# Optimization experiments

Hardware: AMD Instinct MI355X
Metric: run time of the kernel (lower is better)

The kernel has to match this reference:

```python
import jax, jax.numpy as jnp
import numpy as np

C = 1024
B = 32
N = 512
H = W = 32
SUB = (256, 64)
K = (16, 16)
OUT = 3584
LN_EPS = 1e-5


def setup_inputs() -> dict:
    key = jax.random.key(0)
    ks = jax.random.split(key, 12)
    s = 0.02
    C2 = C + 2
    inp = {}
    inp["points"] = jax.random.uniform(ks[0], (B, N, 2), jnp.float32)
    inp["feat_map"] = jax.random.normal(ks[1], (C, H, W), jnp.float32)
    for i in range(2):
        inp[f"diff_w{i}"] = jax.random.normal(ks[2 + 4 * i], (C2, C2), jnp.float32) * s
        inp[f"diff_b{i}"] = jnp.zeros((C2,), jnp.float32)
        inp[f"agg_w{i}"] = jax.random.normal(ks[3 + 4 * i], (C, 2 * C2), jnp.float32) * s
        inp[f"agg_b{i}"] = jnp.zeros((C,), jnp.float32)
        inp[f"ln_g{i}"] = jnp.ones((C,), jnp.float32)
        inp[f"ln_b{i}"] = jnp.zeros((C,), jnp.float32)
    inp["flat_w"] = jax.random.normal(ks[10], (C, C * SUB[-1]), jnp.float32) * s
    inp["flat_b"] = jnp.zeros((C,), jnp.float32)
    inp["dim_w"] = jax.random.normal(ks[11], (OUT, C), jnp.float32) * s
    inp["dim_b"] = jnp.zeros((OUT,), jnp.float32)
    return inp


def _bilinear(feat, xy):
    # feat [C,H,W]; xy [P,2] grid coords in [-1,1], (x,y) order, align_corners=True
    Cc, Hh, Ww = feat.shape
    x = (xy[:, 0] + 1.0) * 0.5 * (Ww - 1)
    y = (xy[:, 1] + 1.0) * 0.5 * (Hh - 1)
    x0 = jnp.floor(x)
    y0 = jnp.floor(y)
    wx = x - x0
    wy = y - y0
    x0i = jnp.clip(x0, 0, Ww - 1).astype(jnp.int32)
    x1i = jnp.clip(x0 + 1, 0, Ww - 1).astype(jnp.int32)
    y0i = jnp.clip(y0, 0, Hh - 1).astype(jnp.int32)
    y1i = jnp.clip(y0 + 1, 0, Hh - 1).astype(jnp.int32)
    f00 = feat[:, y0i, x0i]
    f01 = feat[:, y0i, x1i]
    f10 = feat[:, y1i, x0i]
    f11 = feat[:, y1i, x1i]
    out = (f00 * (1 - wx) * (1 - wy) + f01 * wx * (1 - wy)
           + f10 * (1 - wx) * wy + f11 * wx * wy)
    return out.T  # [P,C]


def _fps(pts, n):
    # iterative farthest point sampling; pts [Np,2] -> indices [n]
    Np = pts.shape[0]

    def body(carry, _):
        dist, far = carry
        d = jnp.sum((pts - pts[far]) ** 2, axis=-1)
        dist = jnp.minimum(dist, d)
        nxt = jnp.argmax(dist).astype(jnp.int32)
        return (dist, nxt), far

    init = (jnp.full((Np,), 1e10, pts.dtype), jnp.int32(0))
    (_, _), idx = jax.lax.scan(body, init, None, length=n)
    return idx


def _stage(points, feats, n_sub, k, dw, db, aw, ab, lg, lb):
    # FPS downsample
    fps_idx = jax.vmap(lambda p: _fps(p, n_sub))(points)              # [B,S]
    new_pts = jnp.take_along_axis(points, fps_idx[..., None], axis=1)  # [B,S,2]
    new_fts = jnp.take_along_axis(feats, fps_idx[..., None], axis=1)   # [B,S,C]
    # brute-force KNN
    d2 = jnp.sum((new_pts[:, :, None, :] - points[:, None, :, :]) ** 2, axis=-1)  # [B,S,N]
    _, nn_idx = jax.lax.top_k(-d2, k)                                   # [B,S,K]
    gp = jax.vmap(lambda p, i: p[i])(points, nn_idx)                    # [B,S,K,2]
    gf = jax.vmap(lambda f, i: f[i])(feats, nn_idx)                     # [B,S,K,C]
    anchor = jnp.concatenate([new_fts, new_pts], axis=-1)[:, :, None, :]  # [B,S,1,C+2]
    diff = jnp.concatenate([gf, gp], axis=-1) - anchor
    diff = diff @ dw.T + db                                             # diff projector
    gath = jnp.concatenate([diff, jnp.broadcast_to(anchor, diff.shape)], axis=-1)  # [B,S,K,2(C+2)]
    h = jax.nn.relu(jnp.einsum('bskd,cd->bskc', gath, aw) + ab)         # 1x1 conv + relu
    mu = jnp.mean(h, axis=-1, keepdims=True)
    var = jnp.var(h, axis=-1, keepdims=True)
    h = (h - mu) * jax.lax.rsqrt(var + LN_EPS) * lg + lb                # layernorm over C
    return new_pts, jnp.max(h, axis=2)                                  # max-pool over neighbors


def _forward(points, feat_map, dw0, db0, aw0, ab0, lg0, lb0,
             dw1, db1, aw1, ab1, lg1, lb1, fw, fb, dmw, dmb):
    Bp, Np = points.shape[0], points.shape[1]
    grid = 2.0 * points[..., ::-1] - 1.0            # flip (row,col) -> (x,y), to [-1,1]
    fts = _bilinear(feat_map, grid.reshape(-1, 2)).reshape(Bp, Np, -1)
    pts = points
    pts, fts = _stage(pts, fts, SUB[0], K[0], dw0, db0, aw0, ab0, lg0, lb0)
    pts, fts = _stage(pts, fts, SUB[1], K[1], dw1, db1, aw1, ab1, lg1, lb1)
    flat = fts.reshape(Bp, -1)
    return (flat @ fw.T + fb) @ dmw.T + dmb


def reference(points, feat_map, diff_w0, diff_b0, agg_w0, agg_b0, ln_g0, ln_b0,
              diff_w1, diff_b1, agg_w1, agg_b1, ln_g1, ln_b1,
              flat_w, flat_b, dim_w, dim_b):
    return _forward(points, feat_map, diff_w0, diff_b0, agg_w0, agg_b0, ln_g0, ln_b0,
                    diff_w1, diff_b1, agg_w1, agg_b1, ln_g1, ln_b1,
                    flat_w, flat_b, dim_w, dim_b)
```

## Files before the change

kernel.cpp:

```cpp
#include <hip/hip_runtime.h>
#include <cstdint>
#include <cstddef>

static const int B_ = 32, N_ = 512, C_ = 1024, C2_ = 1026, CC2_ = 2052;
static const int S0_ = 256, S1_ = 64, K_ = 16, OUT_ = 3584;
static const int LDP_ = 1152;

typedef unsigned short ushort;
typedef __attribute__((ext_vector_type(8))) short short8;
typedef __attribute__((ext_vector_type(4))) float f32x4;

__device__ __forceinline__ ushort f2bf(float x) {
  unsigned u = __float_as_uint(x);
  unsigned r = (u + 0x7fffu + ((u >> 16) & 1u)) >> 16;
  return (ushort)r;
}
__device__ __forceinline__ float bf2f(ushort b) {
  return __uint_as_float(((unsigned)b) << 16);
}

__device__ __forceinline__ void gload16(const void* g, void* l) {
  __builtin_amdgcn_global_load_lds((const __attribute__((address_space(1))) void*)g,
                                   (__attribute__((address_space(3))) void*)l, 16, 0, 0);
}

__device__ __forceinline__ unsigned wave_umax_dpp(unsigned v) {
  unsigned t;
  t = (unsigned)__builtin_amdgcn_update_dpp(0, (int)v, 0x111, 0xf, 0xf, true);
  v = v > t ? v : t;
  t = (unsigned)__builtin_amdgcn_update_dpp(0, (int)v, 0x112, 0xf, 0xf, true);
  v = v > t ? v : t;
  t = (unsigned)__builtin_amdgcn_update_dpp(0, (int)v, 0x114, 0xf, 0xf, true);
  v = v > t ? v : t;
  t = (unsigned)__builtin_amdgcn_update_dpp(0, (int)v, 0x118, 0xf, 0xf, true);
  v = v > t ? v : t;
  t = (unsigned)__builtin_amdgcn_update_dpp(0, (int)v, 0x142, 0xf, 0xf, true);
  v = v > t ? v : t;
  t = (unsigned)__builtin_amdgcn_update_dpp(0, (int)v, 0x143, 0xf, 0xf, true);
  v = v > t ? v : t;
  return v;
}

template <int OMODE>
__device__ __forceinline__ void dev_mgemm(int bx, int by, ushort* As, ushort* Bs, int M, int Neff,
                                          int K, const ushort* __restrict__ A, int lda,
                                          const int* __restrict__ rowidx,
                                          const ushort* __restrict__ Wt, int ldw,
                                          const float* __restrict__ bias,
                                          void* __restrict__ Cout, int ldc) {
  int t = threadIdx.x;
  int w = t >> 6, l = t & 63;
  int row0 = by * 128, col0 = bx * 128;
  f32x4 acc[4][4];
#pragma unroll
  for (int i = 0; i < 4; i++)
#pragma unroll
    for (int j = 0; j < 4; j++) acc[i][j] = (f32x4){0.f, 0.f, 0.f, 0.f};

  int srow = l >> 2;
  int scol = (l & 3) * 8;
  int ar0 = min(row0 + w * 16 + srow, M - 1);
  int ar1 = min(row0 + 64 + w * 16 + srow, M - 1);
  if (rowidx) { ar0 = rowidx[ar0]; ar1 = rowidx[ar1]; }
  const ushort* gA0 = A + (size_t)ar0 * lda + scol;
  const ushort* gA1 = A + (size_t)ar1 * lda + scol;
  const ushort* gB0 = Wt + (size_t)(col0 + w * 16 + srow) * ldw + scol;
  const ushort* gB1 = Wt + (size_t)(col0 + 64 + w * 16 + srow) * ldw + scol;
  ushort* lA0 = As + w * 512;
  ushort* lA1 = As + 2048 + w * 512;
  ushort* lB0 = Bs + w * 512;
  ushort* lB1 = Bs + 2048 + w * 512;

  int wm = w >> 1, wn = w & 1;
  int fr = l & 15, fg = l >> 4;

  for (int kt = 0; kt < K; kt += 64) {
    __syncthreads();
    gload16(gA0 + kt, lA0);
    gload16(gA1 + kt, lA1);
    gload16(gB0 + kt, lB0);
    gload16(gB1 + kt, lB1);
    gload16(gA0 + kt + 32, lA0 + 4096);
    gload16(gA1 + kt + 32, lA1 + 4096);
    gload16(gB0 + kt + 32, lB0 + 4096);
    gload16(gB1 + kt + 32, lB1 + 4096);
    __syncthreads();
#pragma unroll
    for (int ks = 0; ks < 2; ks++) {
      short8 af[4], bf[4];
#pragma unroll
      for (int mi = 0; mi < 4; mi++)
        af[mi] = *(const short8*)&As[ks * 4096 + (wm * 64 + mi * 16 + fr) * 32 + fg * 8];
#pragma unroll
      for (int ni = 0; ni < 4; ni++)
        bf[ni] = *(const short8*)&Bs[ks * 4096 + (wn * 64 + ni * 16 + fr) * 32 + fg * 8];
#pragma unroll
      for (int mi = 0; mi < 4; mi++)
#pragma unroll
        for (int ni = 0; ni < 4; ni++)
          acc[mi][ni] =
              __builtin_amdgcn_mfma_f32_16x16x32_bf16(af[mi], bf[ni], acc[mi][ni], 0, 0, 0);
    }
  }

  ushort* C = (ushort*)Cout;
  if (OMODE == 1) {
#pragma unroll
    for (int mi = 0; mi < 4; mi++)
#pragma unroll
      for (int ni = 0; ni < 4; ni++)
#pragma unroll
        for (int q = 0; q < 4; q++) {
          int r = row0 + wm * 64 + mi * 16 + fg * 4 + q;
          int c = col0 + wn * 64 + ni * 16 + fr;
          if (r < M) C[(size_t)r * ldc + c] = f2bf(c < Neff ? acc[mi][ni][q] : 0.f);
        }
  } else {
#pragma unroll
    for (int mi = 0; mi < 4; mi++)
#pragma unroll
      for (int ni = 0; ni < 4; ni++)
#pragma unroll
        for (int q = 0; q < 4; q++) {
          int r = row0 + wm * 64 + mi * 16 + fg * 4 + q;
          int c = col0 + wn * 64 + ni * 16 + fr;
          if (r < M) C[(size_t)r * ldc + c] = f2bf(acc[mi][ni][q] + bias[c]);
        }
  }
}

template <int NPL>
__device__ __forceinline__ void dev_fps(int b, int Np, int nsub, const float* __restrict__ pts,
                                        int stride, int* __restrict__ rows) {
  __builtin_amdgcn_s_setprio(3);
  int lane = threadIdx.x;
  const float* pb = pts + (size_t)b * Np * stride;
  float px[NPL], py[NPL], dist[NPL];
#pragma unroll
  for (int i = 0; i < NPL; i++) {
    int j = lane + 64 * i;
    px[i] = pb[(size_t)j * stride + 0];
    py[i] = pb[(size_t)j * stride + 1];
    dist[i] = 1e10f;
  }
  int far = 0;
  float fx = pb[0], fy = pb[1];
  for (int s = 0; s < nsub; s++) {
    if (lane == 0) rows[b * nsub + s] = b * Np + far;
    unsigned bd = 0;
    int bidx = lane;
#pragma unroll
    for (int i = 0; i < NPL; i++) {
      float dx = __fsub_rn(px[i], fx), dy = __fsub_rn(py[i], fy);
      float d = __fadd_rn(__fmul_rn(dx, dx), __fmul_rn(dy, dy));
      dist[i] = fminf(dist[i], d);
      unsigned db = __float_as_uint(dist[i]);
      if (i == 0) {
        bd = db;
      } else if (db > bd) {
        bd = db;
        bidx = lane + 64 * i;
      }
    }
    unsigned maxd = (unsigned)__builtin_amdgcn_readlane((int)wave_umax_dpp(bd), 63);
    unsigned cand = (bd == maxd) ? ~(unsigned)bidx : 0u;
    far = (int)~(unsigned)__builtin_amdgcn_readlane((int)wave_umax_dpp(cand), 63);
    int chunk = far >> 6, owner = far & 63;
    float cx = px[0], cy = py[0];
#pragma unroll
    for (int i = 1; i < NPL; i++) {
      bool cnd = (chunk == i);
      cx = cnd ? px[i] : cx;
      cy = cnd ? py[i] : cy;
    }
    fx = __uint_as_float((unsigned)__builtin_amdgcn_readlane((int)__float_as_uint(cx), owner));
    fy = __uint_as_float((unsigned)__builtin_amdgcn_readlane((int)__float_as_uint(cy), owner));
  }
  __builtin_amdgcn_s_setprio(0);
}

template <int NPL>
__device__ __forceinline__ void dev_knn(int bs, int S, int Np, const float* __restrict__ pts,
                                        int stride, const int* __restrict__ rows,
                                        int* __restrict__ nn) {
  int b = bs / S;
  int lane = threadIdx.x & 63;
  const float* pb = pts + (size_t)b * Np * stride;
  int arow = rows[bs];
  float ax = pts[(size_t)arow * stride + 0];
  float ay = pts[(size_t)arow * stride + 1];
  float d2[NPL];
#pragma unroll
  for (int i = 0; i < NPL; i++) {
    int j = lane + 64 * i;
    float dx = __fsub_rn(ax, pb[(size_t)j * stride + 0]);
    float dy = __fsub_rn(ay, pb[(size_t)j * stride + 1]);
    d2[i] = __fadd_rn(__fmul_rn(dx, dx), __fmul_rn(dy, dy));
  }
  unsigned mask = 0;
  for (int k = 0; k < K_; k++) {
    float bv = INFINITY;
    int bi = 0x7fffffff;
#pragma unroll
    for (int i = 0; i < NPL; i++) {
      int j = lane + 64 * i;
      bool used = (mask >> i) & 1u;
      if (!used && (d2[i] < bv || (d2[i] == bv && j < bi))) { bv = d2[i]; bi = j; }
    }
#pragma unroll
    for (int off = 32; off; off >>= 1) {
      float ov = __shfl_xor(bv, off);
      int oi = __shfl_xor(bi, off);
      if (ov < bv || (ov == bv && oi < bi)) { bv = ov; bi = oi; }
    }
    if ((bi & 63) == lane) mask |= 1u << (bi >> 6);
    if (lane == 0) nn[bs * K_ + k] = b * Np + bi;
  }
}

__device__ __forceinline__ void dev_bilinear(int r, const float* __restrict__ points,
                                             const float* __restrict__ fmT,
                                             ushort* __restrict__ X0) {
  float p0 = points[r * 2 + 0], p1 = points[r * 2 + 1];
  float g0 = __fsub_rn(__fmul_rn(2.0f, p1), 1.0f);
  float g1 = __fsub_rn(__fmul_rn(2.0f, p0), 1.0f);
  float x = __fmul_rn(__fmul_rn(__fadd_rn(g0, 1.0f), 0.5f), 31.0f);
  float y = __fmul_rn(__fmul_rn(__fadd_rn(g1, 1.0f), 0.5f), 31.0f);
  float x0f = floorf(x), y0f = floorf(y);
  float wx = __fsub_rn(x, x0f), wy = __fsub_rn(y, y0f);
  int x0i = (int)fminf(fmaxf(x0f, 0.f), 31.f);
  int x1i = (int)fminf(fmaxf(__fadd_rn(x0f, 1.f), 0.f), 31.f);
  int y0i = (int)fminf(fmaxf(y0f, 0.f), 31.f);
  int y1i = (int)fminf(fmaxf(__fadd_rn(y0f, 1.f), 0.f), 31.f);
  float omwx = __fsub_rn(1.f, wx), omwy = __fsub_rn(1.f, wy);
  size_t i00 = (size_t)(y0i * 32 + x0i) * 1024;
  size_t i01 = (size_t)(y0i * 32 + x1i) * 1024;
  size_t i10 = (size_t)(y1i * 32 + x0i) * 1024;
  size_t i11 = (size_t)(y1i * 32 + x1i) * 1024;
  int t = threadIdx.x;
  int c0 = t * 4;
  ushort* xr = X0 + (size_t)r * LDP_;
  float4 f00 = *(const float4*)(fmT + i00 + c0);
  float4 f01 = *(const float4*)(fmT + i01 + c0);
  float4 f10 = *(const float4*)(fmT + i10 + c0);
  float4 f11 = *(const float4*)(fmT + i11 + c0);
  float a[4] = {f00.x, f00.y, f00.z, f00.w};
  float b[4] = {f01.x, f01.y, f01.z, f01.w};
  float c[4] = {f10.x, f10.y, f10.z, f10.w};
  float d[4] = {f11.x, f11.y, f11.z, f11.w};
  ushort o[4];
#pragma unroll
  for (int i = 0; i < 4; i++) {
    float t1 = a[i] * omwx * omwy;
    float t2 = b[i] * wx * omwy;
    float t3 = c[i] * omwx * wy;
    float t4 = d[i] * wx * wy;
    o[i] = f2bf(((t1 + t2) + t3) + t4);
  }
  uint2 uv = {(unsigned)o[0] | ((unsigned)o[1] << 16), (unsigned)o[2] | ((unsigned)o[3] << 16)};
  *(uint2*)(xr + c0) = uv;
  if (t == 0) { xr[1024] = f2bf(p0); xr[1025] = f2bf(p1); }
  if (t < 126) xr[1026 + t] = 0;
}

static const int PREP_CVT = 2304;
static const int PREP_TT = 1296;
static const int PREP_FMT = 1024;
static const int PREP_TOTAL = 4 * PREP_CVT + 2 * PREP_TT + 512 + PREP_FMT;

__global__ __launch_bounds__(256) void k_prep(
    const float* __restrict__ aw0, const float* __restrict__ aw1, const float* __restrict__ dw0,
    const float* __restrict__ dw1, const float* __restrict__ db0, const float* __restrict__ ab0,
    const float* __restrict__ db1, const float* __restrict__ ab1,
    const float* __restrict__ feat_map, ushort* __restrict__ awdb0, ushort* __restrict__ awab0,
    ushort* __restrict__ awdb1, ushort* __restrict__ awab1, ushort* __restrict__ dwT0,
    ushort* __restrict__ dwT1, float* __restrict__ dvp0, float* __restrict__ dvp1,
    float* __restrict__ fmT) {
  __shared__ float tile[32][33];
  int bid = blockIdx.x;
  if (bid < 4 * PREP_CVT) {
    int job = bid / PREP_CVT, lb = bid % PREP_CVT;
    const float* src = (job < 2) ? aw0 : aw1;
    int soff = (job & 1) ? C2_ : 0;
    ushort* dst = (job == 0) ? awdb0 : (job == 1) ? awab0 : (job == 2) ? awdb1 : awab1;
    unsigned e = (lb * 256u + threadIdx.x) * 2u;
    unsigned r = e / (unsigned)LDP_, c = e % (unsigned)LDP_;
    float v0 = 0.f, v1 = 0.f;
    const float* sp = src + (size_t)r * CC2_ + soff + c;
    if ((int)c < C2_) v0 = sp[0];
    if ((int)(c + 1) < C2_) v1 = sp[1];
    *(unsigned*)(dst + e) = (unsigned)f2bf(v0) | ((unsigned)f2bf(v1) << 16);
    return;
  }
  bid -= 4 * PREP_CVT;
  if (bid < 2 * PREP_TT) {
    int which = bid / PREP_TT, id = bid % PREP_TT;
    const float* src = which ? dw1 : dw0;
    ushort* dst = which ? dwT1 : dwT0;
    int bx = (id % 36) * 32, by = (id / 36) * 32;
    int tx = threadIdx.x & 31, ty4 = (threadIdx.x >> 5) * 4;
#pragma unroll
    for (int i = 0; i < 4; i++) {
      int r = by + ty4 + i, c = bx + tx;
      tile[ty4 + i][tx] = (r < C2_ && c < C2_) ? src[(size_t)r * C2_ + c] : 0.f;
    }
    __syncthreads();
#pragma unroll
    for (int i = 0; i < 4; i++)
      dst[(size_t)(bx + ty4 + i) * LDP_ + by + tx] = f2bf(tile[tx][ty4 + i]);
    return;
  }
  bid -= 2 * PREP_TT;
  if (bid < 512) {
    int which = bid >> 8;
    int cb = bid & 255;
    const float* aw = which ? aw1 : aw0;
    const float* db = which ? db1 : db0;
    const float* ab = which ? ab1 : ab0;
    float* dvp = which ? dvp1 : dvp0;
    int w = threadIdx.x >> 6, lane = threadIdx.x & 63;
    int c = cb * 4 + w;
    const float* wr = aw + (size_t)c * CC2_;
    float s = 0.f;
    for (int d = lane; d < C2_; d += 64) s += db[d] * wr[d];
#pragma unroll
    for (int off = 32; off; off >>= 1) s += __shfl_xor(s, off);
    if (lane == 0) dvp[c] = ab[c] + s;
    return;
  }
  bid -= 512;
  {
    int yx0 = (bid & 31) * 32, c0 = (bid >> 5) * 32;
    int tx = threadIdx.x & 31, ty = threadIdx.x >> 5;
#pragma unroll
    for (int i = 0; i < 4; i++)
      tile[ty + 8 * i][tx] = feat_map[(size_t)(c0 + ty + 8 * i) * 1024 + yx0 + tx];
    __syncthreads();
#pragma unroll
    for (int i = 0; i < 4; i++)
      fmT[(size_t)(yx0 + ty + 8 * i) * 1024 + c0 + tx] = tile[tx][ty + 8 * i];
  }
}

__global__ __launch_bounds__(256) void k_wc_bil(
    const ushort* __restrict__ awdb0, const ushort* __restrict__ dwT0, ushort* __restrict__ Wcb0,
    const ushort* __restrict__ awdb1, const ushort* __restrict__ dwT1, ushort* __restrict__ Wcb1,
    const float* __restrict__ points, const float* __restrict__ fmT, ushort* __restrict__ Xb0) {
  __shared__ ushort As[8192];
  __shared__ ushort Bs[8192];
  int bid = blockIdx.x;
  if (bid < 72) {
    dev_mgemm<1>(bid / 8, bid % 8, As, Bs, C_, C2_, LDP_, awdb0, LDP_, nullptr, dwT0, LDP_,
                 nullptr, Wcb0, LDP_);
  } else if (bid < 144) {
    int b2 = bid - 72;
    dev_mgemm<1>(b2 / 8, b2 % 8, As, Bs, C_, C2_, LDP_, awdb1, LDP_, nullptr, dwT1, LDP_, nullptr,
                 Wcb1, LDP_);
  } else {
    dev_bilinear(bid - 144, points, fmT, Xb0);
  }
}

template <int NPL>
__global__ __launch_bounds__(256) void k_gemm_fps(int nrb, int Mg, const ushort* __restrict__ A,
                                                  int lda, const ushort* __restrict__ Wt,
                                                  ushort* __restrict__ Gout, int Np, int nsub,
                                                  const float* __restrict__ pts, int stride,
                                                  int* __restrict__ rows) {
  __shared__ ushort As[8192];
  __shared__ ushort Bs[8192];
  int bid = blockIdx.x;
  if (bid < 32) {
    if (threadIdx.x < 64) dev_fps<NPL>(bid, Np, nsub, pts, stride, rows);
    return;
  }
  int b2 = bid - 32;
  dev_mgemm<1>(b2 / nrb, b2 % nrb, As, Bs, Mg, C_, LDP_, A, lda, nullptr, Wt, LDP_, nullptr, Gout,
               C_);
}

template <int NPL>
__global__ __launch_bounds__(256) void k_gemm_knn(int nrb, int Mp, const ushort* __restrict__ A,
                                                  int lda, const int* __restrict__ rowsA,
                                                  const ushort* __restrict__ Wt,
                                                  const float* __restrict__ bias,
                                                  ushort* __restrict__ Pout, int ngemm, int S,
                                                  int Np, const float* __restrict__ pts,
                                                  int stride, const int* __restrict__ rows,
                                                  int* __restrict__ nn) {
  __shared__ ushort As[8192];
  __shared__ ushort Bs[8192];
  int bid = blockIdx.x;
  if (bid < ngemm) {
    dev_mgemm<2>(bid / nrb, bid % nrb, As, Bs, Mp, C_, LDP_, A, lda, rowsA, Wt, LDP_, bias, Pout,
                 C_);
  } else {
    int w = threadIdx.x >> 6;
    int qid = (bid - ngemm) * 4 + w;
    dev_knn<NPL>(qid, S, Np, pts, stride, rows, nn);
  }
}

__global__ __launch_bounds__(256) void k_flat(const ushort* __restrict__ A,
                                              const float* __restrict__ W,
                                              float* __restrict__ Cp) {
  int t = threadIdx.x;
  int w = t >> 6, l = t & 63;
  int fr = l & 15, fg = l >> 4;
  int col0 = blockIdx.x * 128 + w * 32;
  size_t k0 = (size_t)blockIdx.z * 2048;
  f32x4 acc[2][2];
#pragma unroll
  for (int i = 0; i < 2; i++)
#pragma unroll
    for (int j = 0; j < 2; j++) acc[i][j] = (f32x4){0.f, 0.f, 0.f, 0.f};
  const ushort* a0 = A + (size_t)fr * 65536 + k0 + fg * 8;
  const ushort* a1 = A + (size_t)(16 + fr) * 65536 + k0 + fg * 8;
  const float* b0 = W + (size_t)(col0 + fr) * 65536 + k0 + fg * 8;
  const float* b1 = W + (size_t)(col0 + 16 + fr) * 65536 + k0 + fg * 8;
  for (int kt = 0; kt < 2048; kt += 32) {
    short8 af0 = *(const short8*)(a0 + kt);
    short8 af1 = *(const short8*)(a1 + kt);
    float4 p0 = *(const float4*)(b0 + kt);
    float4 p1 = *(const float4*)(b0 + kt + 4);
    float4 q0 = *(const float4*)(b1 + kt);
    float4 q1 = *(const float4*)(b1 + kt + 4);
    short8 bf0, bf1;
    bf0[0] = (short)f2bf(p0.x); bf0[1] = (short)f2bf(p0.y);
    bf0[2] = (short)f2bf(p0.z); bf0[3] = (short)f2bf(p0.w);
    bf0[4] = (short)f2bf(p1.x); bf0[5] = (short)f2bf(p1.y);
    bf0[6] = (short)f2bf(p1.z); bf0[7] = (short)f2bf(p1.w);
    bf1[0] = (short)f2bf(q0.x); bf1[1] = (short)f2bf(q0.y);
    bf1[2] = (short)f2bf(q0.z); bf1[3] = (short)f2bf(q0.w);
    bf1[4] = (short)f2bf(q1.x); bf1[5] = (short)f2bf(q1.y);
    bf1[6] = (short)f2bf(q1.z); bf1[7] = (short)f2bf(q1.w);
    acc[0][0] = __builtin_amdgcn_mfma_f32_16x16x32_bf16(af0, bf0, acc[0][0], 0, 0, 0);
    acc[1][0] = __builtin_amdgcn_mfma_f32_16x16x32_bf16(af1, bf0, acc[1][0], 0, 0, 0);
    acc[0][1] = __builtin_amdgcn_mfma_f32_16x16x32_bf16(af0, bf1, acc[0][1], 0, 0, 0);
    acc[1][1] = __builtin_amdgcn_mfma_f32_16x16x32_bf16(af1, bf1, acc[1][1], 0, 0, 0);
  }
  float* Cz = Cp + (size_t)blockIdx.z * 32 * 1024;
#pragma unroll
  for (int mi = 0; mi < 2; mi++)
#pragma unroll
    for (int ni = 0; ni < 2; ni++)
#pragma unroll
      for (int q = 0; q < 4; q++) {
        int r = mi * 16 + fg * 4 + q;
        int c = col0 + ni * 16 + fr;
        Cz[(size_t)r * 1024 + c] = acc[mi][ni][q];
      }
}

__global__ __launch_bounds__(256) void k_dim(const ushort* __restrict__ A,
                                             const float* __restrict__ W,
                                             float* __restrict__ Cp) {
  int t = threadIdx.x;
  int w = t >> 6, l = t & 63;
  int fr = l & 15, fg = l >> 4;
  int col0 = blockIdx.x * 128 + w * 32;
  int k0 = blockIdx.z * 256;
  f32x4 acc[2][2];
#pragma unroll
  for (int i = 0; i < 2; i++)
#pragma unroll
    for (int j = 0; j < 2; j++) acc[i][j] = (f32x4){0.f, 0.f, 0.f, 0.f};
  const ushort* a0 = A + (size_t)fr * 1024 + k0 + fg * 8;
  const ushort* a1 = A + (size_t)(16 + fr) * 1024 + k0 + fg * 8;
  const float* b0 = W + (size_t)(col0 + fr) * 1024 + k0 + fg * 8;
  const float* b1 = W + (size_t)(col0 + 16 + fr) * 1024 + k0 + fg * 8;
  for (int kt = 0; kt < 256; kt += 32) {
    short8 af0 = *(const short8*)(a0 + kt);
    short8 af1 = *(const short8*)(a1 + kt);
    float4 p0 = *(const float4*)(b0 + kt);
    float4 p1 = *(const float4*)(b0 + kt + 4);
    float4 q0 = *(const float4*)(b1 + kt);
    float4 q1 = *(const float4*)(b1 + kt + 4);
    short8 bf0, bf1;
    bf0[0] = (short)f2bf(p0.x); bf0[1] = (short)f2bf(p0.y);
    bf0[2] = (short)f2bf(p0.z); bf0[3] = (short)f2bf(p0.w);
    bf0[4] = (short)f2bf(p1.x); bf0[5] = (short)f2bf(p1.y);
    bf0[6] = (short)f2bf(p1.z); bf0[7] = (short)f2bf(p1.w);
    bf1[0] = (short)f2bf(q0.x); bf1[1] = (short)f2bf(q0.y);
    bf1[2] = (short)f2bf(q0.z); bf1[3] = (short)f2bf(q0.w);
    bf1[4] = (short)f2bf(q1.x); bf1[5] = (short)f2bf(q1.y);
    bf1[6] = (short)f2bf(q1.z); bf1[7] = (short)f2bf(q1.w);
    acc[0][0] = __builtin_amdgcn_mfma_f32_16x16x32_bf16(af0, bf0, acc[0][0], 0, 0, 0);
    acc[1][0] = __builtin_amdgcn_mfma_f32_16x16x32_bf16(af1, bf0, acc[1][0], 0, 0, 0);
    acc[0][1] = __builtin_amdgcn_mfma_f32_16x16x32_bf16(af0, bf1, acc[0][1], 0, 0, 0);
    acc[1][1] = __builtin_amdgcn_mfma_f32_16x16x32_bf16(af1, bf1, acc[1][1], 0, 0, 0);
  }
  float* Cz = Cp + (size_t)blockIdx.z * 32 * 3584;
#pragma unroll
  for (int mi = 0; mi < 2; mi++)
#pragma unroll
    for (int ni = 0; ni < 2; ni++)
#pragma unroll
      for (int q = 0; q < 4; q++) {
        int r = mi * 16 + fg * 4 + q;
        int c = col0 + ni * 16 + fr;
        Cz[(size_t)r * 3584 + c] = acc[mi][ni][q];
      }
}

__global__ __launch_bounds__(256) void k_fused_stage(
    const ushort* __restrict__ G, const ushort* __restrict__ Pb, const int* __restrict__ rows,
    const int* __restrict__ nn, const float* __restrict__ lng, const float* __restrict__ lnb,
    const float* __restrict__ prev_pts, int pts_stride, ushort* __restrict__ Xout, int ld_out,
    float* __restrict__ coords_out) {
  __shared__ float sm[4][1024];
  int chunk = (int)gridDim.x >> 3;
  int bs = (blockIdx.x & 7) * chunk + (blockIdx.x >> 3);
  int t = threadIdx.x;
  int w = t >> 6, lane = t & 63;
  int c0 = lane * 16;
  int arow = rows[bs];
  float base[16], lg[16], lb[16], acc[16];
  {
    short8 pA = *(const short8*)(Pb + (size_t)bs * C_ + c0);
    short8 pB = *(const short8*)(Pb + (size_t)bs * C_ + c0 + 8);
    short8 gA = *(const short8*)(G + (size_t)arow * C_ + c0);
    short8 gB = *(const short8*)(G + (size_t)arow * C_ + c0 + 8);
#pragma unroll
    for (int i = 0; i < 8; i++) {
      base[i] = bf2f((ushort)pA[i]) - bf2f((ushort)gA[i]);
      base[8 + i] = bf2f((ushort)pB[i]) - bf2f((ushort)gB[i]);
    }
#pragma unroll
    for (int i = 0; i < 4; i++) {
      float4 gv = *(const float4*)(lng + c0 + 4 * i);
      float4 bv = *(const float4*)(lnb + c0 + 4 * i);
      lg[4 * i] = gv.x; lg[4 * i + 1] = gv.y; lg[4 * i + 2] = gv.z; lg[4 * i + 3] = gv.w;
      lb[4 * i] = bv.x; lb[4 * i + 1] = bv.y; lb[4 * i + 2] = bv.z; lb[4 * i + 3] = bv.w;
      acc[4 * i] = -INFINITY; acc[4 * i + 1] = -INFINITY;
      acc[4 * i + 2] = -INFINITY; acc[4 * i + 3] = -INFINITY;
    }
  }
#pragma unroll
  for (int kk = 0; kk < 4; kk++) {
    int g = nn[bs * K_ + w * 4 + kk];
    const ushort* Gr = G + (size_t)g * C_ + c0;
    short8 xA = *(const short8*)(Gr);
    short8 xB = *(const short8*)(Gr + 8);
    float v[16];
    float s1 = 0.f, s2 = 0.f;
#pragma unroll
    for (int i = 0; i < 8; i++) {
      float x = fmaxf(bf2f((ushort)xA[i]) + base[i], 0.f);
      v[i] = x; s1 += x; s2 += x * x;
      float y = fmaxf(bf2f((ushort)xB[i]) + base[8 + i], 0.f);
      v[8 + i] = y; s1 += y; s2 += y * y;
    }
#pragma unroll
    for (int off = 32; off; off >>= 1) {
      s1 += __shfl_xor(s1, off);
      s2 += __shfl_xor(s2, off);
    }
    float mu = s1 * (1.f / 1024.f);
    float var = s2 * (1.f / 1024.f) - mu * mu;
    float rstd = 1.f / sqrtf(var + 1e-5f);
#pragma unroll
    for (int i = 0; i < 16; i++) {
      float nv = (v[i] - mu) * rstd * lg[i] + lb[i];
      acc[i] = fmaxf(acc[i], nv);
    }
  }
#pragma unroll
  for (int i = 0; i < 16; i += 4) {
    f32x4 av = {acc[i], acc[i + 1], acc[i + 2], acc[i + 3]};
    *(f32x4*)&sm[w][c0 + i] = av;
  }
  __syncthreads();
  {
    int cc = t * 4;
    f32x4 m0 = *(const f32x4*)&sm[0][cc];
    f32x4 m1 = *(const f32x4*)&sm[1][cc];
    f32x4 m2 = *(const f32x4*)&sm[2][cc];
    f32x4 m3 = *(const f32x4*)&sm[3][cc];
    ushort o[4];
#pragma unroll
    for (int j = 0; j < 4; j++)
      o[j] = f2bf(fmaxf(fmaxf(m0[j], m1[j]), fmaxf(m2[j], m3[j])));
    uint2 uv = {(unsigned)o[0] | ((unsigned)o[1] << 16), (unsigned)o[2] | ((unsigned)o[3] << 16)};
    *(uint2*)(Xout + (size_t)bs * ld_out + cc) = uv;
  }
  if (prev_pts) {
    float p0 = prev_pts[(size_t)arow * pts_stride + 0];
    float p1 = prev_pts[(size_t)arow * pts_stride + 1];
    if (t == 0) {
      Xout[(size_t)bs * ld_out + 1024] = f2bf(p0);
      Xout[(size_t)bs * ld_out + 1025] = f2bf(p1);
      coords_out[bs * 2 + 0] = p0;
      coords_out[bs * 2 + 1] = p1;
    }
    if (t < 126) Xout[(size_t)bs * ld_out + 1026 + t] = 0;
  }
}

template <int OUTBF>
__global__ __launch_bounds__(256) void k_reduce(int total, int Ncols, int nz,
                                                const float* __restrict__ part,
                                                const float* __restrict__ bias,
                                                void* __restrict__ out) {
  int i = blockIdx.x * 256 + threadIdx.x;
  if (i >= total) return;
  float s = bias[i % Ncols];
  for (int z = 0; z < nz; z++) s += part[(size_t)z * total + i];
  if (OUTBF)
    ((ushort*)out)[i] = f2bf(s);
  else
    ((float*)out)[i] = s;
}

extern "C" void kernel_launch(void* const* d_in, const int* in_sizes, int n_in, void* d_out,
                              int out_size, void* d_ws, size_t ws_size, hipStream_t stream) {
  (void)in_sizes; (void)n_in; (void)out_size; (void)ws_size;
  const float* points = (const float*)d_in[0];
  const float* feat_map = (const float*)d_in[1];
  const float* dw0 = (const float*)d_in[2];
  const float* db0 = (const float*)d_in[3];
  const float* aw0 = (const float*)d_in[4];
  const float* ab0 = (const float*)d_in[5];
  const float* lg0 = (const float*)d_in[6];
  const float* lb0 = (const float*)d_in[7];
  const float* dw1 = (const float*)d_in[8];
  const float* db1 = (const float*)d_in[9];
  const float* aw1 = (const float*)d_in[10];
  const float* ab1 = (const float*)d_in[11];
  const float* lg1 = (const float*)d_in[12];
  const float* lb1 = (const float*)d_in[13];
  const float* fw = (const float*)d_in[14];
  const float* fb = (const float*)d_in[15];
  const float* dmw = (const float*)d_in[16];
  const float* dmb = (const float*)d_in[17];
  float* out = (float*)d_out;

  char* wsb = (char*)d_ws;
  size_t off = 0;
  auto alloc = [&](size_t bytes) -> void* {
    void* p = wsb + off;
    off = (off + bytes + 255) & ~(size_t)255;
    return p;
  };
  float* fmT = (float*)alloc((size_t)1024 * 1024 * 4);
  ushort* Xb0 = (ushort*)alloc((size_t)B_ * N_ * LDP_ * 2);
  ushort* Gb = (ushort*)alloc((size_t)B_ * N_ * C_ * 2);
  ushort* Pb = (ushort*)alloc((size_t)B_ * S0_ * C_ * 2);
  ushort* Xb1 = (ushort*)alloc((size_t)B_ * S0_ * LDP_ * 2);
  ushort* fts2b = (ushort*)alloc((size_t)B_ * S1_ * C_ * 2);
  float* coords1 = (float*)alloc((size_t)B_ * S0_ * 2 * 4);
  ushort* awdb0 = (ushort*)alloc((size_t)C_ * LDP_ * 2);
  ushort* awab0 = (ushort*)alloc((size_t)C_ * LDP_ * 2);
  ushort* awdb1 = (ushort*)alloc((size_t)C_ * LDP_ * 2);
  ushort* awab1 = (ushort*)alloc((size_t)C_ * LDP_ * 2);
  ushort* dwT0 = (ushort*)alloc((size_t)LDP_ * LDP_ * 2);
  ushort* dwT1 = (ushort*)alloc((size_t)LDP_ * LDP_ * 2);
  ushort* Wcb0 = (ushort*)alloc((size_t)C_ * LDP_ * 2);
  ushort* Wcb1 = (ushort*)alloc((size_t)C_ * LDP_ * 2);
  float* dvp0 = (float*)alloc(1024 * 4);
  float* dvp1 = (float*)alloc(1024 * 4);
  int* rows0 = (int*)alloc(B_ * S0_ * 4);
  int* nn0 = (int*)alloc(B_ * S0_ * K_ * 4);
  int* rows1 = (int*)alloc(B_ * S1_ * 4);
  int* nn1 = (int*)alloc(B_ * S1_ * K_ * 4);
  float* hpart = (float*)alloc((size_t)32 * B_ * C_ * 4);
  ushort* hidb = (ushort*)alloc((size_t)B_ * C_ * 2);
  float* opart = (float*)alloc((size_t)4 * B_ * OUT_ * 4);

  k_prep<<<PREP_TOTAL, 256, 0, stream>>>(aw0, aw1, dw0, dw1, db0, ab0, db1, ab1, feat_map, awdb0,
                                         awab0, awdb1, awab1, dwT0, dwT1, dvp0, dvp1, fmT);
  k_wc_bil<<<144 + B_ * N_, 256, 0, stream>>>(awdb0, dwT0, Wcb0, awdb1, dwT1, Wcb1, points, fmT,
                                              Xb0);
  k_gemm_fps<8><<<32 + 1024, 256, 0, stream>>>(128, B_ * N_, Xb0, LDP_, Wcb0, Gb, N_, S0_, points,
                                               2, rows0);
  k_gemm_knn<8><<<512 + (B_ * S0_) / 4, 256, 0, stream>>>(64, B_ * S0_, Xb0, LDP_, rows0, awab0,
                                                          dvp0, Pb, 512, S0_, N_, points, 2,
                                                          rows0, nn0);
  k_fused_stage<<<B_ * S0_, 256, 0, stream>>>(Gb, Pb, rows0, nn0, lg0, lb0, points, 2, Xb1, LDP_,
                                              coords1);
  k_gemm_fps<4><<<32 + 512, 256, 0, stream>>>(64, B_ * S0_, Xb1, LDP_, Wcb1, Gb, S0_, S1_,
                                              coords1, 2, rows1);
  k_gemm_knn<4><<<128 + (B_ * S1_) / 4, 256, 0, stream>>>(16, B_ * S1_, Xb1, LDP_, rows1, awab1,
                                                          dvp1, Pb, 128, S1_, S0_, coords1, 2,
                                                          rows1, nn1);
  k_fused_stage<<<B_ * S1_, 256, 0, stream>>>(Gb, Pb, rows1, nn1, lg1, lb1, nullptr, 0, fts2b, C_,
                                              nullptr);
  {
    dim3 g(8, 1, 32);
    k_flat<<<g, 256, 0, stream>>>(fts2b, fw, hpart);
  }
  k_reduce<1><<<(B_ * C_ + 255) / 256, 256, 0, stream>>>(B_ * C_, C_, 32, hpart, fb, hidb);
  {
    dim3 g(28, 1, 4);
    k_dim<<<g, 256, 0, stream>>>(hidb, dmw, opart);
  }
  k_reduce<0><<<(B_ * OUT_ + 255) / 256, 256, 0, stream>>>(B_ * OUT_, OUT_, 4, opart, dmb, out);
}
```

Baseline: 474.0 us.

## Pre-convert flat_w to bf16 inside stage-0 kernels and drop k_dim split-K

Adds extra blocks to the stage-0 gemm_fps and gemm_knn launches that convert the 256 MB fp32 flat_w into a 128 MB bf16 workspace copy. k_flat can then stream half the bytes from that copy, and the conversion overlaps with the latency-bound FPS/KNN work. Separately, k_dim no longer splits K four ways; it writes out directly with the bias added, which removes the partial buffer and the final reduce launch. The cost is an extra full read of flat_w plus a bf16 write each call, and k_dim now runs on only 28 blocks.

```diff
diff --git a/kernel.cpp b/kernel.cpp
--- a/kernel.cpp
+++ b/kernel.cpp
@@ -39,6 +39,19 @@
   t = (unsigned)__builtin_amdgcn_update_dpp(0, (int)v, 0x143, 0xf, 0xf, true);
   v = v > t ? v : t;
   return v;
+}
+
+__device__ __forceinline__ void dev_cvt_fw(int cb, const float* __restrict__ src,
+                                           ushort* __restrict__ dst) {
+  size_t base = (size_t)cb * 32768 + threadIdx.x * 4;
+#pragma unroll
+  for (int i = 0; i < 32; i++) {
+    size_t e = base + (size_t)i * 1024;
+    float4 v = *(const float4*)(src + e);
+    uint2 u = {(unsigned)f2bf(v.x) | ((unsigned)f2bf(v.y) << 16),
+               (unsigned)f2bf(v.z) | ((unsigned)f2bf(v.w) << 16)};
+    *(uint2*)(dst + e) = u;
+  }
 }
 
 template <int OMODE>
@@ -362,11 +375,14 @@
 }
 
 template <int NPL>
-__global__ __launch_bounds__(256) void k_gemm_fps(int nrb, int Mg, const ushort* __restrict__ A,
-                                                  int lda, const ushort* __restrict__ Wt,
+__global__ __launch_bounds__(256) void k_gemm_fps(int nrb, int ngemm, int Mg,
+                                                  const ushort* __restrict__ A, int lda,
+                                                  const ushort* __restrict__ Wt,
                                                   ushort* __restrict__ Gout, int Np, int nsub,
                                                   const float* __restrict__ pts, int stride,
-                                                  int* __restrict__ rows) {
+                                                  int* __restrict__ rows,
+                                                  const float* __restrict__ fwsrc,
+                                                  ushort* __restrict__ fwdst, int cvt0) {
   __shared__ ushort As[8192];
   __shared__ ushort Bs[8192];
   int bid = blockIdx.x;
@@ -375,8 +391,12 @@
     return;
   }
   int b2 = bid - 32;
-  dev_mgemm<1>(b2 / nrb, b2 % nrb, As, Bs, Mg, C_, LDP_, A, lda, nullptr, Wt, LDP_, nullptr, Gout,
-               C_);
+  if (b2 < ngemm) {
+    dev_mgemm<1>(b2 / nrb, b2 % nrb, As, Bs, Mg, C_, LDP_, A, lda, nullptr, Wt, LDP_, nullptr,
+                 Gout, C_);
+    return;
+  }
+  dev_cvt_fw(cvt0 + b2 - ngemm, fwsrc, fwdst);
 }
 
 template <int NPL>
@@ -384,25 +404,32 @@
                                                   int lda, const int* __restrict__ rowsA,
                                                   const ushort* __restrict__ Wt,
                                                   const float* __restrict__ bias,
-                                                  ushort* __restrict__ Pout, int ngemm, int S,
-                                                  int Np, const float* __restrict__ pts,
+                                                  ushort* __restrict__ Pout, int ngemm, int nknnb,
+                                                  int S, int Np, const float* __restrict__ pts,
                                                   int stride, const int* __restrict__ rows,
-                                                  int* __restrict__ nn) {
+                                                  int* __restrict__ nn,
+                                                  const float* __restrict__ fwsrc,
+                                                  ushort* __restrict__ fwdst, int cvt0) {
   __shared__ ushort As[8192];
   __shared__ ushort Bs[8192];
   int bid = blockIdx.x;
   if (bid < ngemm) {
     dev_mgemm<2>(bid / nrb, bid % nrb, As, Bs, Mp, C_, LDP_, A, lda, rowsA, Wt, LDP_, bias, Pout,
                  C_);
-  } else {
+    return;
+  }
+  if (bid < ngemm + nknnb) {
     int w = threadIdx.x >> 6;
     int qid = (bid - ngemm) * 4 + w;
     dev_knn<NPL>(qid, S, Np, pts, stride, rows, nn);
-  }
-}
-
+    return;
+  }
+  dev_cvt_fw(cvt0 + bid - ngemm - nknnb, fwsrc, fwdst);
+}
+
+template <int WBF>
 __global__ __launch_bounds__(256) void k_flat(const ushort* __restrict__ A,
-                                              const float* __restrict__ W,
+                                              const void* __restrict__ W,
                                               float* __restrict__ Cp) {
   int t = threadIdx.x;
   int w = t >> 6, l = t & 63;
@@ -416,9 +443,75 @@
     for (int j = 0; j < 2; j++) acc[i][j] = (f32x4){0.f, 0.f, 0.f, 0.f};
   const ushort* a0 = A + (size_t)fr * 65536 + k0 + fg * 8;
   const ushort* a1 = A + (size_t)(16 + fr) * 65536 + k0 + fg * 8;
-  const float* b0 = W + (size_t)(col0 + fr) * 65536 + k0 + fg * 8;
-  const float* b1 = W + (size_t)(col0 + 16 + fr) * 65536 + k0 + fg * 8;
-  for (int kt = 0; kt < 2048; kt += 32) {
+  if (WBF) {
+    const ushort* b0 = (const ushort*)W + (size_t)(col0 + fr) * 65536 + k0 + fg * 8;
+    const ushort* b1 = (const ushort*)W + (size_t)(col0 + 16 + fr) * 65536 + k0 + fg * 8;
+    for (int kt = 0; kt < 2048; kt += 32) {
+      short8 af0 = *(const short8*)(a0 + kt);
+      short8 af1 = *(const short8*)(a1 + kt);
+      short8 bf0 = *(const short8*)(b0 + kt);
+      short8 bf1 = *(const short8*)(b1 + kt);
+      acc[0][0] = __builtin_amdgcn_mfma_f32_16x16x32_bf16(af0, bf0, acc[0][0], 0, 0, 0);
+      acc[1][0] = __builtin_amdgcn_mfma_f32_16x16x32_bf16(af1, bf0, acc[1][0], 0, 0, 0);
+      acc[0][1] = __builtin_amdgcn_mfma_f32_16x16x32_bf16(af0, bf1, acc[0][1], 0, 0, 0);
+      acc[1][1] = __builtin_amdgcn_mfma_f32_16x16x32_bf16(af1, bf1, acc[1][1], 0, 0, 0);
+    }
+  } else {
+    const float* b0 = (const float*)W + (size_t)(col0 + fr) * 65536 + k0 + fg * 8;
+    const float* b1 = (const float*)W + (size_t)(col0 + 16 + fr) * 65536 + k0 + fg * 8;
+    for (int kt = 0; kt < 2048; kt += 32) {
+      short8 af0 = *(const short8*)(a0 + kt);
+      short8 af1 = *(const short8*)(a1 + kt);
+      float4 p0 = *(const float4*)(b0 + kt);
+      float4 p1 = *(const float4*)(b0 + kt + 4);
+      float4 q0 = *(const float4*)(b1 + kt);
+      float4 q1 = *(const float4*)(b1 + kt + 4);
+      short8 bf0, bf1;
+      bf0[0] = (short)f2bf(p0.x); bf0[1] = (short)f2bf(p0.y);
+      bf0[2] = (short)f2bf(p0.z); bf0[3] = (short)f2bf(p0.w);
+      bf0[4] = (short)f2bf(p1.x); bf0[5] = (short)f2bf(p1.y);
+      bf0[6] = (short)f2bf(p1.z); bf0[7] = (short)f2bf(p1.w);
+      bf1[0] = (short)f2bf(q0.x); bf1[1] = (short)f2bf(q0.y);
+      bf1[2] = (short)f2bf(q0.z); bf1[3] = (short)f2bf(q0.w);
+      bf1[4] = (short)f2bf(q1.x); bf1[5] = (short)f2bf(q1.y);
+      bf1[6] = (short)f2bf(q1.z); bf1[7] = (short)f2bf(q1.w);
+      acc[0][0] = __builtin_amdgcn_mfma_f32_16x16x32_bf16(af0, bf0, acc[0][0], 0, 0, 0);
+      acc[1][0] = __builtin_amdgcn_mfma_f32_16x16x32_bf16(af1, bf0, acc[1][0], 0, 0, 0);
+      acc[0][1] = __builtin_amdgcn_mfma_f32_16x16x32_bf16(af0, bf1, acc[0][1], 0, 0, 0);
+      acc[1][1] = __builtin_amdgcn_mfma_f32_16x16x32_bf16(af1, bf1, acc[1][1], 0, 0, 0);
+    }
+  }
+  float* Cz = Cp + (size_t)blockIdx.z * 32 * 1024;
+#pragma unroll
+  for (int mi = 0; mi < 2; mi++)
+#pragma unroll
+    for (int ni = 0; ni < 2; ni++)
+#pragma unroll
+      for (int q = 0; q < 4; q++) {
+        int r = mi * 16 + fg * 4 + q;
+        int c = col0 + ni * 16 + fr;
+        Cz[(size_t)r * 1024 + c] = acc[mi][ni][q];
+      }
+}
+
+__global__ __launch_bounds__(256) void k_dim(const ushort* __restrict__ A,
+                                             const float* __restrict__ W,
+                                             const float* __restrict__ bias,
+                                             float* __restrict__ outp) {
+  int t = threadIdx.x;
+  int w = t >> 6, l = t & 63;
+  int fr = l & 15, fg = l >> 4;
+  int col0 = blockIdx.x * 128 + w * 32;
+  f32x4 acc[2][2];
+#pragma unroll
+  for (int i = 0; i < 2; i++)
+#pragma unroll
+    for (int j = 0; j < 2; j++) acc[i][j] = (f32x4){0.f, 0.f, 0.f, 0.f};
+  const ushort* a0 = A + (size_t)fr * 1024 + fg * 8;
+  const ushort* a1 = A + (size_t)(16 + fr) * 1024 + fg * 8;
+  const float* b0 = W + (size_t)(col0 + fr) * 1024 + fg * 8;
+  const float* b1 = W + (size_t)(col0 + 16 + fr) * 1024 + fg * 8;
+  for (int kt = 0; kt < 1024; kt += 32) {
     short8 af0 = *(const short8*)(a0 + kt);
     short8 af1 = *(const short8*)(a1 + kt);
     float4 p0 = *(const float4*)(b0 + kt);
@@ -439,7 +532,6 @@
     acc[0][1] = __builtin_amdgcn_mfma_f32_16x16x32_bf16(af0, bf1, acc[0][1], 0, 0, 0);
     acc[1][1] = __builtin_amdgcn_mfma_f32_16x16x32_bf16(af1, bf1, acc[1][1], 0, 0, 0);
   }
-  float* Cz = Cp + (size_t)blockIdx.z * 32 * 1024;
 #pragma unroll
   for (int mi = 0; mi < 2; mi++)
 #pragma unroll
@@ -448,58 +540,7 @@
       for (int q = 0; q < 4; q++) {
         int r = mi * 16 + fg * 4 + q;
         int c = col0 + ni * 16 + fr;
-        Cz[(size_t)r * 1024 + c] = acc[mi][ni][q];
-      }
-}
-
-__global__ __launch_bounds__(256) void k_dim(const ushort* __restrict__ A,
-                                             const float* __restrict__ W,
-                                             float* __restrict__ Cp) {
-  int t = threadIdx.x;
-  int w = t >> 6, l = t & 63;
-  int fr = l & 15, fg = l >> 4;
-  int col0 = blockIdx.x * 128 + w * 32;
-  int k0 = blockIdx.z * 256;
-  f32x4 acc[2][2];
-#pragma unroll
-  for (int i = 0; i < 2; i++)
-#pragma unroll
-    for (int j = 0; j < 2; j++) acc[i][j] = (f32x4){0.f, 0.f, 0.f, 0.f};
-  const ushort* a0 = A + (size_t)fr * 1024 + k0 + fg * 8;
-  const ushort* a1 = A + (size_t)(16 + fr) * 1024 + k0 + fg * 8;
-  const float* b0 = W + (size_t)(col0 + fr) * 1024 + k0 + fg * 8;
-  const float* b1 = W + (size_t)(col0 + 16 + fr) * 1024 + k0 + fg * 8;
-  for (int kt = 0; kt < 256; kt += 32) {
-    short8 af0 = *(const short8*)(a0 + kt);
-    short8 af1 = *(const short8*)(a1 + kt);
-    float4 p0 = *(const float4*)(b0 + kt);
-    float4 p1 = *(const float4*)(b0 + kt + 4);
-    float4 q0 = *(const float4*)(b1 + kt);
-    float4 q1 = *(const float4*)(b1 + kt + 4);
-    short8 bf0, bf1;
-    bf0[0] = (short)f2bf(p0.x); bf0[1] = (short)f2bf(p0.y);
-    bf0[2] = (short)f2bf(p0.z); bf0[3] = (short)f2bf(p0.w);
-    bf0[4] = (short)f2bf(p1.x); bf0[5] = (short)f2bf(p1.y);
-    bf0[6] = (short)f2bf(p1.z); bf0[7] = (short)f2bf(p1.w);
-    bf1[0] = (short)f2bf(q0.x); bf1[1] = (short)f2bf(q0.y);
-    bf1[2] = (short)f2bf(q0.z); bf1[3] = (short)f2bf(q0.w);
-    bf1[4] = (short)f2bf(q1.x); bf1[5] = (short)f2bf(q1.y);
-    bf1[6] = (short)f2bf(q1.z); bf1[7] = (short)f2bf(q1.w);
-    acc[0][0] = __builtin_amdgcn_mfma_f32_16x16x32_bf16(af0, bf0, acc[0][0], 0, 0, 0);
-    acc[1][0] = __builtin_amdgcn_mfma_f32_16x16x32_bf16(af1, bf0, acc[1][0], 0, 0, 0);
-    acc[0][1] = __builtin_amdgcn_mfma_f32_16x16x32_bf16(af0, bf1, acc[0][1], 0, 0, 0);
-    acc[1][1] = __builtin_amdgcn_mfma_f32_16x16x32_bf16(af1, bf1, acc[1][1], 0, 0, 0);
-  }
-  float* Cz = Cp + (size_t)blockIdx.z * 32 * 3584;
-#pragma unroll
-  for (int mi = 0; mi < 2; mi++)
-#pragma unroll
-    for (int ni = 0; ni < 2; ni++)
-#pragma unroll
-      for (int q = 0; q < 4; q++) {
-        int r = mi * 16 + fg * 4 + q;
-        int c = col0 + ni * 16 + fr;
-        Cz[(size_t)r * 3584 + c] = acc[mi][ni][q];
+        outp[(size_t)r * 3584 + c] = acc[mi][ni][q] + bias[c];
       }
 }
 
@@ -614,7 +655,7 @@
 
 extern "C" void kernel_launch(void* const* d_in, const int* in_sizes, int n_in, void* d_out,
                               int out_size, void* d_ws, size_t ws_size, hipStream_t stream) {
-  (void)in_sizes; (void)n_in; (void)out_size; (void)ws_size;
+  (void)in_sizes; (void)n_in; (void)out_size;
   const float* points = (const float*)d_in[0];
   const float* feat_map = (const float*)d_in[1];
   const float* dw0 = (const float*)d_in[2];
@@ -665,34 +706,40 @@
   int* nn1 = (int*)alloc(B_ * S1_ * K_ * 4);
   float* hpart = (float*)alloc((size_t)32 * B_ * C_ * 4);
   ushort* hidb = (ushort*)alloc((size_t)B_ * C_ * 2);
-  float* opart = (float*)alloc((size_t)4 * B_ * OUT_ * 4);
+  ushort* fwb = (ushort*)alloc((size_t)C_ * 65536 * 2);
+  bool use_fwb = (off <= ws_size);
 
   k_prep<<<PREP_TOTAL, 256, 0, stream>>>(aw0, aw1, dw0, dw1, db0, ab0, db1, ab1, feat_map, awdb0,
                                          awab0, awdb1, awab1, dwT0, dwT1, dvp0, dvp1, fmT);
   k_wc_bil<<<144 + B_ * N_, 256, 0, stream>>>(awdb0, dwT0, Wcb0, awdb1, dwT1, Wcb1, points, fmT,
                                               Xb0);
-  k_gemm_fps<8><<<32 + 1024, 256, 0, stream>>>(128, B_ * N_, Xb0, LDP_, Wcb0, Gb, N_, S0_, points,
-                                               2, rows0);
-  k_gemm_knn<8><<<512 + (B_ * S0_) / 4, 256, 0, stream>>>(64, B_ * S0_, Xb0, LDP_, rows0, awab0,
-                                                          dvp0, Pb, 512, S0_, N_, points, 2,
-                                                          rows0, nn0);
+  {
+    int ncvt = use_fwb ? 1024 : 0;
+    k_gemm_fps<8><<<32 + 1024 + ncvt, 256, 0, stream>>>(128, 1024, B_ * N_, Xb0, LDP_, Wcb0, Gb,
+                                                        N_, S0_, points, 2, rows0, fw, fwb, 0);
+  }
+  {
+    int ncvt = use_fwb ? 1024 : 0;
+    k_gemm_knn<8><<<512 + 2048 + ncvt, 256, 0, stream>>>(64, B_ * S0_, Xb0, LDP_, rows0, awab0,
+                                                         dvp0, Pb, 512, 2048, S0_, N_, points, 2,
+                                                         rows0, nn0, fw, fwb, 1024);
+  }
   k_fused_stage<<<B_ * S0_, 256, 0, stream>>>(Gb, Pb, rows0, nn0, lg0, lb0, points, 2, Xb1, LDP_,
                                               coords1);
-  k_gemm_fps<4><<<32 + 512, 256, 0, stream>>>(64, B_ * S0_, Xb1, LDP_, Wcb1, Gb, S0_, S1_,
-                                              coords1, 2, rows1);
-  k_gemm_knn<4><<<128 + (B_ * S1_) / 4, 256, 0, stream>>>(16, B_ * S1_, Xb1, LDP_, rows1, awab1,
-                                                          dvp1, Pb, 128, S1_, S0_, coords1, 2,
-                                                          rows1, nn1);
+  k_gemm_fps<4><<<32 + 512, 256, 0, stream>>>(64, 512, B_ * S0_, Xb1, LDP_, Wcb1, Gb, S0_, S1_,
+                                              coords1, 2, rows1, nullptr, nullptr, 0);
+  k_gemm_knn<4><<<128 + 512, 256, 0, stream>>>(16, B_ * S1_, Xb1, LDP_, rows1, awab1, dvp1, Pb,
+                                               128, 512, S1_, S0_, coords1, 2, rows1, nn1,
+                                               nullptr, nullptr, 0);
   k_fused_stage<<<B_ * S1_, 256, 0, stream>>>(Gb, Pb, rows1, nn1, lg1, lb1, nullptr, 0, fts2b, C_,
                                               nullptr);
   {
     dim3 g(8, 1, 32);
-    k_flat<<<g, 256, 0, stream>>>(fts2b, fw, hpart);
+    if (use_fwb)
+      k_flat<1><<<g, 256, 0, stream>>>(fts2b, fwb, hpart);
+    else
+      k_flat<0><<<g, 256, 0, stream>>>(fts2b, fw, hpart);
   }
   k_reduce<1><<<(B_ * C_ + 255) / 256, 256, 0, stream>>>(B_ * C_, C_, 32, hpart, fb, hidb);
-  {
-    dim3 g(28, 1, 4);
-    k_dim<<<g, 256, 0, stream>>>(hidb, dmw, opart);
-  }
-  k_reduce<0><<<(B_ * OUT_ + 255) / 256, 256, 0, stream>>>(B_ * OUT_, OUT_, 4, opart, dmb, out);
-}
+  k_dim<<<28, 256, 0, stream>>>(hidb, dmw, dmb, out);
+}
```

New measurement: 529.7 us. +11.8%, slower.

## Move stage-0 FPS earlier and merge stage-0 GEMMs with KNN; trim K padding

Applied to the files above, without the earlier changes.

Stage-0 farthest point sampling now runs inside the weight-combine/bilinear kernel, so the two stage-0 GEMMs and the KNN can share a single launch (k_stage0) instead of two. This removes a kernel launch and the serial dependency between them. Separately, every GEMM now iterates over an effective K of 1088 instead of the padded 1152, skipping zero-padded columns. The risk is correctness if the padding between 1088 and 1152 is not zero, or if the padded region holds the bias column.

```diff
diff --git a/kernel.cpp b/kernel.cpp
--- a/kernel.cpp
+++ b/kernel.cpp
@@ -5,6 +5,7 @@
 static const int B_ = 32, N_ = 512, C_ = 1024, C2_ = 1026, CC2_ = 2052;
 static const int S0_ = 256, S1_ = 64, K_ = 16, OUT_ = 3584;
 static const int LDP_ = 1152;
+static const int KEFF_ = 1088;
 
 typedef unsigned short ushort;
 typedef __attribute__((ext_vector_type(8))) short short8;
@@ -345,20 +346,50 @@
 __global__ __launch_bounds__(256) void k_wc_bil(
     const ushort* __restrict__ awdb0, const ushort* __restrict__ dwT0, ushort* __restrict__ Wcb0,
     const ushort* __restrict__ awdb1, const ushort* __restrict__ dwT1, ushort* __restrict__ Wcb1,
-    const float* __restrict__ points, const float* __restrict__ fmT, ushort* __restrict__ Xb0) {
+    const float* __restrict__ points, const float* __restrict__ fmT, ushort* __restrict__ Xb0,
+    int* __restrict__ rows0) {
   __shared__ ushort As[8192];
   __shared__ ushort Bs[8192];
   int bid = blockIdx.x;
+  if (bid < 32) {
+    if (threadIdx.x < 64) dev_fps<8>(bid, N_, S0_, points, 2, rows0);
+    return;
+  }
+  bid -= 32;
   if (bid < 72) {
-    dev_mgemm<1>(bid / 8, bid % 8, As, Bs, C_, C2_, LDP_, awdb0, LDP_, nullptr, dwT0, LDP_,
+    dev_mgemm<1>(bid / 8, bid % 8, As, Bs, C_, C2_, KEFF_, awdb0, LDP_, nullptr, dwT0, LDP_,
                  nullptr, Wcb0, LDP_);
   } else if (bid < 144) {
     int b2 = bid - 72;
-    dev_mgemm<1>(b2 / 8, b2 % 8, As, Bs, C_, C2_, LDP_, awdb1, LDP_, nullptr, dwT1, LDP_, nullptr,
+    dev_mgemm<1>(b2 / 8, b2 % 8, As, Bs, C_, C2_, KEFF_, awdb1, LDP_, nullptr, dwT1, LDP_, nullptr,
                  Wcb1, LDP_);
   } else {
     dev_bilinear(bid - 144, points, fmT, Xb0);
   }
+}
+
+__global__ __launch_bounds__(256) void k_stage0(
+    const ushort* __restrict__ Xb0, const ushort* __restrict__ Wcb0, ushort* __restrict__ Gb,
+    const int* __restrict__ rows0, const ushort* __restrict__ awab0,
+    const float* __restrict__ dvp0, ushort* __restrict__ Pb, const float* __restrict__ points,
+    int* __restrict__ nn0) {
+  __shared__ ushort As[8192];
+  __shared__ ushort Bs[8192];
+  int bid = blockIdx.x;
+  if (bid < 1024) {
+    dev_mgemm<1>(bid / 128, bid % 128, As, Bs, B_ * N_, C_, KEFF_, Xb0, LDP_, nullptr, Wcb0, LDP_,
+                 nullptr, Gb, C_);
+    return;
+  }
+  if (bid < 1536) {
+    int b2 = bid - 1024;
+    dev_mgemm<2>(b2 / 64, b2 % 64, As, Bs, B_ * S0_, C_, KEFF_, Xb0, LDP_, rows0, awab0, LDP_,
+                 dvp0, Pb, C_);
+    return;
+  }
+  int w = threadIdx.x >> 6;
+  int qid = (bid - 1536) * 4 + w;
+  dev_knn<8>(qid, S0_, N_, points, 2, rows0, nn0);
 }
 
 template <int NPL>
@@ -375,8 +406,8 @@
     return;
   }
   int b2 = bid - 32;
-  dev_mgemm<1>(b2 / nrb, b2 % nrb, As, Bs, Mg, C_, LDP_, A, lda, nullptr, Wt, LDP_, nullptr, Gout,
-               C_);
+  dev_mgemm<1>(b2 / nrb, b2 % nrb, As, Bs, Mg, C_, KEFF_, A, lda, nullptr, Wt, LDP_, nullptr,
+               Gout, C_);
 }
 
 template <int NPL>
@@ -392,7 +423,7 @@
   __shared__ ushort Bs[8192];
   int bid = blockIdx.x;
   if (bid < ngemm) {
-    dev_mgemm<2>(bid / nrb, bid % nrb, As, Bs, Mp, C_, LDP_, A, lda, rowsA, Wt, LDP_, bias, Pout,
+    dev_mgemm<2>(bid / nrb, bid % nrb, As, Bs, Mp, C_, KEFF_, A, lda, rowsA, Wt, LDP_, bias, Pout,
                  C_);
   } else {
     int w = threadIdx.x >> 6;
@@ -669,13 +700,9 @@
 
   k_prep<<<PREP_TOTAL, 256, 0, stream>>>(aw0, aw1, dw0, dw1, db0, ab0, db1, ab1, feat_map, awdb0,
                                          awab0, awdb1, awab1, dwT0, dwT1, dvp0, dvp1, fmT);
-  k_wc_bil<<<144 + B_ * N_, 256, 0, stream>>>(awdb0, dwT0, Wcb0, awdb1, dwT1, Wcb1, points, fmT,
-                                              Xb0);
-  k_gemm_fps<8><<<32 + 1024, 256, 0, stream>>>(128, B_ * N_, Xb0, LDP_, Wcb0, Gb, N_, S0_, points,
-                                               2, rows0);
-  k_gemm_knn<8><<<512 + (B_ * S0_) / 4, 256, 0, stream>>>(64, B_ * S0_, Xb0, LDP_, rows0, awab0,
-                                                          dvp0, Pb, 512, S0_, N_, points, 2,
-                                                          rows0, nn0);
+  k_wc_bil<<<32 + 144 + B_ * N_, 256, 0, stream>>>(awdb0, dwT0, Wcb0, awdb1, dwT1, Wcb1, points,
+                                                   fmT, Xb0, rows0);
+  k_stage0<<<3584, 256, 0, stream>>>(Xb0, Wcb0, Gb, rows0, awab0, dvp0, Pb, points, nn0);
   k_fused_stage<<<B_ * S0_, 256, 0, stream>>>(Gb, Pb, rows0, nn0, lg0, lb0, points, 2, Xb1, LDP_,
                                               coords1);
   k_gemm_fps<4><<<32 + 512, 256, 0, stream>>>(64, B_ * S0_, Xb1, LDP_, Wcb1, Gb, S0_, S1_,
```

Measured after the change: 471.8 us. Within noise of the previous version (-0.5%).
